# Kernel tuning notes

Measured on AMD Instinct MI355X. Metric: run time of the kernel, lower is better.

## Reference

```python
import jax, jax.numpy as jnp
import numpy as np
from jax.scipy.special import gammaln

EPS = 1e-8
N_SAMPLES = 2 ** 17
ATTACK_FULL_SIZE = 2048
CPD = 16
N_RES = 16
EXPR = 2
N_OSC = 2
N_GAUSS = 8
N_EVENTS = 4
FRAMES = 128
DEF_FRAMES = 128
N_LEVELS = 11  # log2(ATTACK_FULL_SIZE)


def unit_norm(x, axis=-1):
    return x / (jnp.linalg.norm(x, axis=axis, keepdims=True) + EPS)


def fft_convolve(a, b):
    # zero-pad to 2n to avoid circular wraparound, multiply spectra, crop to n
    n = a.shape[-1]
    fa = jnp.fft.rfft(a, n=2 * n, axis=-1)
    fb = jnp.fft.rfft(b, n=2 * n, axis=-1)
    return jnp.fft.irfft(fa * fb, n=2 * n, axis=-1)[..., :n]


def upsample_with_holes(x, size):
    # zero-insertion upsampling: place frames at stride `factor`
    factor = size // x.shape[-1]
    out = jnp.zeros(x.shape[:-1] + (size,), x.dtype)
    return out.at[..., ::factor].set(x)


def interpolate_last_axis(x, size):
    # linear interpolation, align_corners=False semantics (torch F.interpolate)
    n = x.shape[-1]
    scale = n / size
    src = jnp.clip((jnp.arange(size) + 0.5) * scale - 0.5, 0.0, n - 1.0)
    lo = jnp.floor(src).astype(jnp.int32)
    hi = jnp.minimum(lo + 1, n - 1)
    w = (src - lo).astype(x.dtype)
    return x[..., lo] * (1.0 - w) + x[..., hi] * w


def ensure_last_axis_length(x, size):
    n = x.shape[-1]
    if n == size:
        return x
    if n > size:
        return x[..., :size]
    return jnp.pad(x, [(0, 0)] * (x.ndim - 1) + [(0, size - n)])


def sparse_softmax(x):
    # hard one-hot forward, softmax straight-through backward
    sm = jax.nn.softmax(x, axis=-1)
    hard = jax.nn.one_hot(jnp.argmax(x, axis=-1), x.shape[-1], dtype=x.dtype)
    return hard + sm - jax.lax.stop_gradient(sm)


def hierarchical_dirac(p):
    # p: (..., L, 2) binary choices per level -> one-hot dirac of length 2**L
    sel = sparse_softmax(p)
    sig = sel[..., 0, :]
    for i in range(1, p.shape[-2]):
        sig = (sig[..., :, None] * sel[..., i, :][..., None, :]).reshape(*sig.shape[:-1], -1)
    return sig


def gamma_pdf(mean, std, n_elements):
    # gamma pdf on support (eps, 1], parameterized by mean/std
    t = jnp.linspace(EPS, 1.0, n_elements)
    k = (mean / (std + EPS)) ** 2
    rate = mean / (std ** 2 + EPS)
    k = k[..., None]
    rate = rate[..., None]
    logp = k * jnp.log(rate + EPS) + (k - 1.0) * jnp.log(t) - rate * t - gammaln(k)
    return jnp.exp(logp)


def damped_harmonic_oscillator(time, mass, damping, tension, x0):
    # underdamped closed-form solution, v0 = 0
    omega0_sq = tension / mass
    gamma = damping / (2.0 * mass)
    omega = jnp.sqrt(omega0_sq - gamma ** 2)
    A = x0
    B = gamma * x0 / omega
    return jnp.exp(-gamma * time) * (A * jnp.cos(omega * time) + B * jnp.sin(omega * time))


def dho_block(damping, mass, tension, disp, amps, tmod=None, scaling=None):
    time = jnp.linspace(0.0, 10.0, N_SAMPLES).reshape(1, 1, 1, N_SAMPLES)
    t = tension[..., None]  # (N_OSC, N_RES, EXPR, 1)
    if tmod is not None:
        t = t + tmod[0] * scaling  # broadcast -> (N_OSC, N_RES, EXPR, N_SAMPLES)
    x = damped_harmonic_oscillator(
        time,
        jax.nn.sigmoid(mass[..., None]) * 2.0,
        jax.nn.sigmoid(damping[..., None]) * 30.0,
        10.0 ** t,
        disp[..., None],
    )
    x = (x * amps).sum(axis=0)  # sum over oscillators
    return x.reshape(1, 1, N_RES, EXPR, N_SAMPLES)


def attack_envelopes(means, stds, amps, pos, overall_amp):
    m, s, a = jnp.abs(means), jnp.abs(stds), jnp.abs(amps)
    p = hierarchical_dirac(pos)  # (1,1,CPD,NG,2048)
    x = gamma_pdf(m, s, ATTACK_FULL_SIZE) * a[..., None]
    x = fft_convolve(x, p)
    x = x.sum(axis=2)  # (1,1,NG,2048)
    x = unit_norm(x)
    x = x * overall_amp[..., None]  # broadcast -> (1,1,CPD,NG,2048)
    x = x.sum(axis=-2)  # (1,1,CPD,2048)
    return x.reshape(CPD, ATTACK_FULL_SIZE)


def _forward(control_signal, deformations, ae_means, ae_stds, ae_amps, ae_pos,
             ae_overall_amp, dho_damping, dho_mass, dho_tension, dho_disp, dho_amp,
             influences, stack_mix, router, layer_mix, gains, attack_noise):
    b, ne, cpd, frames = control_signal.shape
    # --- DampedHarmonicOscillatorStack ---
    o1 = dho_block(dho_damping[0], dho_mass[0], dho_tension[0], dho_disp[0], dho_amp[0])
    o2 = dho_block(dho_damping[1], dho_mass[1], dho_tension[1], dho_disp[1], dho_amp[1], o1, influences[0])
    o3 = dho_block(dho_damping[2], dho_mass[2], dho_tension[2], dho_disp[2], dho_amp[2], o2, influences[1])
    res = (jnp.stack([o1, o2, o3], axis=-1) * jax.nn.softmax(stack_mix, axis=-1)).sum(axis=-1)
    res = unit_norm(res)
    # --- AttackEnvelopes ---
    ae = attack_envelopes(ae_means, ae_stds, ae_amps, ae_pos, ae_overall_amp)
    # --- execute_layer ---
    routed = jnp.einsum('becf,cr->berf', control_signal, router)
    before = routed
    res = unit_norm(res)  # execute_layer normalizes again
    routed = upsample_with_holes(routed.reshape(b, ne, N_RES, 1, frames), N_SAMPLES)
    # ae.shape[-1] == window_size, so materialize_attack_envelopes just multiplies noise
    impulse = ensure_last_axis_length(ae * attack_noise, N_SAMPLES).reshape(1, 1, cpd, 1, N_SAMPLES)
    routed = fft_convolve(impulse, routed)  # (1,ne,N_RES,1,S)
    cs = routed.reshape(1, ne, cpd, N_SAMPLES).sum(axis=1, keepdims=True)
    conv = fft_convolve(routed, res)  # (1,ne,N_RES,EXPR,S)
    base = jnp.zeros_like(deformations).at[:, :, 0:1, :].set(1.0)
    d = jax.nn.softmax(base + deformations, axis=-2)
    d = interpolate_last_axis(d.reshape(b, 1, 1, EXPR, -1), N_SAMPLES)
    x = (d * conv).sum(axis=-2)  # (1,ne,N_RES,S)
    mixes = jax.nn.softmax(layer_mix.reshape(1, 1, N_RES, 1, 1, 2), axis=-1)
    stacked = jnp.stack([routed, x.reshape(routed.shape)], axis=-1)
    x = (mixes * stacked).sum(axis=-1)
    x = x.reshape(1, 1, N_RES, -1)
    summed = jnp.tanh(x * jnp.abs(gains.reshape(1, 1, N_RES, 1)))
    summed = summed.sum(axis=-2, keepdims=True)
    return summed, before, cs


def setup_inputs() -> dict:
    key = jax.random.key(0)
    ks = jax.random.split(key, 20)
    u = lambda k, shape, lo, hi: jax.random.uniform(k, shape, jnp.float32, lo, hi)
    inp = {}
    inp['control_signal'] = jax.random.uniform(ks[0], (1, N_EVENTS, CPD, FRAMES), jnp.float32)
    inp['deformations'] = jax.random.normal(ks[1], (1, 1, EXPR, DEF_FRAMES), jnp.float32)
    inp['ae_means'] = u(ks[2], (1, 1, CPD, N_GAUSS), -6.0, 6.0)
    inp['ae_stds'] = u(ks[3], (1, 1, CPD, N_GAUSS), 0.5, 6.0)
    inp['ae_amps'] = u(ks[4], (1, 1, CPD, N_GAUSS), -6.0, 6.0)
    inp['ae_pos'] = u(ks[5], (1, 1, CPD, N_GAUSS, N_LEVELS, 2), -1.0, 1.0)
    inp['ae_overall_amp'] = u(ks[6], (1, 1, CPD, 1), -1.0, 1.0)
    inp['dho_damping'] = u(ks[7], (3, N_OSC, N_RES, EXPR), 0.5, 1.5)
    inp['dho_mass'] = u(ks[8], (3, N_OSC, N_RES, EXPR), -2.0, 2.0)
    inp['dho_tension'] = u(ks[9], (3, N_OSC, N_RES, EXPR), 4.0, 9.0)
    inp['dho_disp'] = u(ks[10], (3, N_OSC, N_RES, EXPR), -1.0, 2.0)
    inp['dho_amp'] = u(ks[11], (3, N_OSC, N_RES, EXPR, 1), -1.0, 1.0)
    inp['influences'] = u(ks[12], (2, N_OSC, N_RES, EXPR, 1), -0.01, 0.01)
    inp['stack_mix'] = u(ks[13], (1, 1, N_RES, EXPR, 1, 3), -1.0, 1.0)
    router = u(ks[14], (CPD, N_RES), -1.0, 1.0)
    mask = (jax.random.uniform(ks[15], (CPD, N_RES)) < 0.1).astype(jnp.float32)
    inp['router'] = router * mask
    inp['layer_mix'] = u(ks[16], (N_RES, 2), -1.0, 1.0)
    inp['gains'] = u(ks[17], (N_RES, 1), 0.01, 1.1)
    inp['attack_noise'] = u(ks[18], (CPD, ATTACK_FULL_SIZE), -1.0, 1.0)
    return inp


def reference(control_signal, deformations, ae_means, ae_stds, ae_amps, ae_pos,
              ae_overall_amp, dho_damping, dho_mass, dho_tension, dho_disp, dho_amp,
              influences, stack_mix, router, layer_mix, gains, attack_noise):
    return _forward(control_signal, deformations, ae_means, ae_stds, ae_amps, ae_pos,
                    ae_overall_amp, dho_damping, dho_mass, dho_tension, dho_disp, dho_amp,
                    influences, stack_mix, router, layer_mix, gains, attack_noise)
```

## Files before the change

### kernel.cpp

```cpp
#include <hip/hip_runtime.h>
#include <math.h>

#define NS 131072
#define EPSF 1e-8f

#define OFF_IMP    8388608u
#define OFF_VG     8421376u
#define OFF_DW     8437760u
#define OFF_FV     8568832u
#define OFF_NORM   8577024u
#define OFF_MIX0   8577064u
#define OFF_MIX1   8577080u
#define OFF_GABS   8577096u
#define OFF_PART   8578560u
#define OFF_GSSP   8594944u

#define AFRAG_USH  4194304u
#define ABF2_USH   4726784u
#define HB_USH     8388608u

typedef __attribute__((ext_vector_type(8))) short short8;
typedef __attribute__((ext_vector_type(4))) float floatx4;
typedef __attribute__((ext_vector_type(4))) unsigned short ushort4v;

#define INV2PI 0.15915494309189535f

__device__ __forceinline__ float sigmf(float x) { return 1.0f / (1.0f + expf(-x)); }

__device__ __forceinline__ unsigned short f2bf(float x) {
  unsigned u = __float_as_uint(x);
  unsigned r = (u + 0x7FFFu + ((u >> 16) & 1u)) >> 16;
  return (unsigned short)r;
}

__global__ __launch_bounds__(256) void k01_prep_dho(
    const float* __restrict__ csig, const float* __restrict__ deform,
    const float* __restrict__ ddmp, const float* __restrict__ dmas,
    const float* __restrict__ dten, const float* __restrict__ ddisp,
    const float* __restrict__ damp, const float* __restrict__ infl,
    const float* __restrict__ smix, const float* __restrict__ router,
    const float* __restrict__ lmix, const float* __restrict__ gains,
    const float* __restrict__ means, const float* __restrict__ stds,
    const float* __restrict__ amps, const float* __restrict__ pos,
    float* __restrict__ wsf, unsigned short* __restrict__ abf2,
    unsigned short* __restrict__ resb, float* __restrict__ partials,
    float* __restrict__ out)
{
  int tid = threadIdx.x;
  int bid = blockIdx.x;
  if (bid < 512) {
    int t = bid * 256 + tid;
    {
      float4 z = {0.f, 0.f, 0.f, 0.f};
      *(float4*)&out[(size_t)t * 4] = z;
    }
    {
      float src = (t + 0.5f) * (1.0f / 1024.0f) - 0.5f;
      src = fminf(fmaxf(src, 0.0f), 127.0f);
      int lo = (int)src;
      int hi = min(lo + 1, 127);
      float w = src - (float)lo;
      float c0l = 1.0f / (1.0f + expf(deform[128 + lo] - (1.0f + deform[lo])));
      float c0h = 1.0f / (1.0f + expf(deform[128 + hi] - (1.0f + deform[hi])));
      wsf[OFF_DW + t] = c0l * (1.0f - w) + c0h * w;
    }
    int mt = bid & 7, e = (bid >> 3) & 3, r = (bid >> 5) & 15;
    __shared__ float fvrow[128];
    if (tid < 128) {
      float s = 0.f;
      for (int c = 0; c < 16; ++c)
        s += csig[(e * 16 + c) * 128 + tid] * router[c * 16 + r];
      fvrow[tid] = s;
      if (mt == 0) {
        wsf[OFF_FV + (e * 16 + r) * 128 + tid] = s;
        out[524288 + (e * 16 + r) * 128 + tid] = s;
      }
    }
    __syncthreads();
    {
      int gid = bid * 256 + tid;
      int lane = gid & 63;
      int kt = (gid >> 6) & 3;
      int m = lane & 15, quad = lane >> 4;
      int base = mt * 16 + m - kt * 32 - quad * 8;
      short8 v;
#pragma unroll
      for (int j = 0; j < 8; ++j) {
        int f = base - j;
        unsigned short b = 0;
        if (f >= 0 && f < 128) b = f2bf(fvrow[f]);
        v[j] = (short)b;
      }
      *(short8*)&abf2[(size_t)gid * 8] = v;
    }
    if (bid == 0 && tid < 16) {
      int r2 = tid;
      float l0 = lmix[r2 * 2], l1 = lmix[r2 * 2 + 1];
      float mx = fmaxf(l0, l1);
      float e0 = expf(l0 - mx), e1 = expf(l1 - mx), inv = 1.0f / (e0 + e1);
      wsf[OFF_MIX0 + r2] = e0 * inv;
      wsf[OFF_MIX1 + r2] = e1 * inv;
      wsf[OFF_GABS + r2] = fabsf(gains[r2]);
    }
  } else if (bid < 576) {
    int gb = bid - 512;
    int g = gb >> 3;
    int i = (gb & 7) * 256 + tid;
    __shared__ float kS[16], rateS[16], logAS[16], aS[16];
    __shared__ int dS[16];
    __shared__ float red[4];
    if (tid < 16) {
      int c = tid, idx = c * 8 + g;
      double m = fabs((double)means[idx]);
      double s = fabs((double)stds[idx]);
      double k = m / (s + 1e-8); k = k * k;
      double rate = m / (s * s + 1e-8);
      double logA = k * log(rate + 1e-8) - lgamma(k);
      kS[c] = (float)k; rateS[c] = (float)rate; logAS[c] = (float)logA;
      aS[c] = fabsf(amps[idx]);
      int d = 0;
      for (int l = 0; l < 11; ++l) {
        float p0 = pos[(idx * 11 + l) * 2], p1 = pos[(idx * 11 + l) * 2 + 1];
        d = d * 2 + (p1 > p0 ? 1 : 0);
      }
      dS[c] = d;
    }
    __syncthreads();
    const float step = (float)((1.0 - 1e-8) / 2047.0);
    float v = 0.f;
    for (int c = 0; c < 16; ++c) {
      int mi = i - dS[c];
      if (mi >= 0) {
        float tm = 1e-8f + (float)mi * step;
        float lp = logAS[c] + (kS[c] - 1.0f) * __logf(tm) - rateS[c] * tm;
        v += aS[c] * __expf(lp);
      }
    }
    wsf[OFF_VG + g * 2048 + i] = v;
    float sumsq = v * v;
#pragma unroll
    for (int off = 32; off; off >>= 1) sumsq += __shfl_down(sumsq, off, 64);
    if ((tid & 63) == 0) red[tid >> 6] = sumsq;
    __syncthreads();
    if (tid == 0) wsf[OFF_GSSP + gb] = red[0] + red[1] + red[2] + red[3];
  } else {
    int b = bid - 576;
    int rx = b >> 9;
    int t = (b & 511) * 256 + tid;
    int r = rx >> 1, x = rx & 1;
    __shared__ float pf[40];
    __shared__ float bred[4];
    if (tid < 6) {
      int ent = tid, bb = ent >> 1, o = ent & 1;
      int id = ((bb * 2 + o) * 16 + r) * 2 + x;
      float mass = 2.0f * sigmf(dmas[id]);
      float gam = 30.0f * sigmf(ddmp[id]) / (2.0f * mass);
      double W = exp((double)dten[id] * 2.302585092994046) / (double)mass;
      float x0v = ddisp[id];
      float ampv = damp[id];
      float infv = 0.f;
      if (bb == 1) infv = infl[(o * 16 + r) * 2 + x];
      if (bb == 2) infv = infl[((2 + o) * 16 + r) * 2 + x];
      pf[0 + ent]  = -gam;
      pf[6 + ent]  = ampv * x0v;
      pf[12 + ent] = gam * ampv * x0v;
      pf[18 + ent] = infv * 2.3025851f;
      if (bb == 0) {
        double om = sqrt(W - (double)gam * (double)gam);
        pf[24 + o] = (float)((double)(gam * x0v * ampv) / om);
        pf[26 + o] = (float)(om * 0.15915494309189535);
      } else {
        pf[28 + ent - 2] = (float)W;
      }
    }
    if (tid == 8) {
      float a0 = smix[rx * 3], a1 = smix[rx * 3 + 1], a2 = smix[rx * 3 + 2];
      float mm = fmaxf(a0, fmaxf(a1, a2));
      float e0 = expf(a0 - mm), e1 = expf(a1 - mm), e2 = expf(a2 - mm);
      float inv = 1.0f / (e0 + e1 + e2);
      pf[33] = e0 * inv; pf[34] = e1 * inv; pf[35] = e2 * inv;
    }
    __syncthreads();
    float ttf = (float)t * (10.0f / 131071.0f);
    float o1v = 0.f;
#pragma unroll
    for (int o = 0; o < 2; ++o) {
      float fr = pf[26 + o] * ttf;
      fr -= rintf(fr);
      float sn = __builtin_amdgcn_sinf(fr);
      float cn = __builtin_amdgcn_cosf(fr);
      float ex = __expf(pf[o] * ttf);
      o1v += ex * (pf[6 + o] * cn + pf[24 + o] * sn);
    }
    float prev = o1v, o2v = 0.f, o3v = 0.f;
#pragma unroll
    for (int blk = 1; blk < 3; ++blk) {
      float acc = 0.f;
#pragma unroll
      for (int oo = 0; oo < 2; ++oo) {
        int o = blk * 2 + oo;
        float ng = pf[o];
        float p10 = __expf(prev * pf[18 + o]);
        float rad = __builtin_fmaf(pf[28 + o - 2], p10, -(ng * ng));
        float om = __builtin_amdgcn_sqrtf(rad);
        float fr = (om * INV2PI) * ttf;
        fr -= rintf(fr);
        float sn = __builtin_amdgcn_sinf(fr);
        float cn = __builtin_amdgcn_cosf(fr);
        float Bp = pf[12 + o] * __builtin_amdgcn_rcpf(om);
        float ex = __expf(ng * ttf);
        acc += ex * (pf[6 + o] * cn + Bp * sn);
      }
      if (blk == 1) o2v = acc; else o3v = acc;
      prev = acc;
    }
    float rv = pf[33] * o1v + pf[34] * o2v + pf[35] * o3v;
    resb[(size_t)rx * NS + t] = f2bf(rv);
    float sq = rv * rv;
#pragma unroll
    for (int off = 32; off; off >>= 1) sq += __shfl_down(sq, off, 64);
    if ((tid & 63) == 0) bred[tid >> 6] = sq;
    __syncthreads();
    if (tid == 0)
      partials[rx * 512 + (b & 511)] = bred[0] + bred[1] + bred[2] + bred[3];
  }
}

__global__ __launch_bounds__(256) void kB_mid(
    const float* __restrict__ ovamp, const float* __restrict__ noise,
    float* __restrict__ wsf, unsigned short* __restrict__ abf)
{
  int bid = blockIdx.x;
  int tid = threadIdx.x;
  if (bid < 32) {
    int rx = bid;
    const float* partials = wsf + OFF_PART;
    __shared__ float red[4];
    float s = partials[rx * 512 + tid] + partials[rx * 512 + 256 + tid];
#pragma unroll
    for (int off = 32; off; off >>= 1) s += __shfl_down(s, off, 64);
    if ((tid & 63) == 0) red[tid >> 6] = s;
    __syncthreads();
    if (tid == 0) wsf[OFF_NORM + rx] = red[0] + red[1] + red[2] + red[3];
    return;
  }
  __shared__ float wS[8];
  if (tid < 8) {
    float g8 = 0.f;
#pragma unroll
    for (int u = 0; u < 8; ++u) g8 += wsf[OFF_GSSP + tid * 8 + u];
    wS[tid] = 1.0f / (sqrtf(g8) + EPSF);
  }
  __syncthreads();
  const float* vg = wsf + OFF_VG;
  if (bid < 160) {
    int idx0 = bid - 32;
    int c = idx0 >> 3;
    int i = (idx0 & 7) * 256 + tid;
    float S = 0.f;
#pragma unroll
    for (int g = 0; g < 8; ++g) S += vg[g * 2048 + i] * wS[g];
    wsf[OFF_IMP + c * 2048 + i] = ovamp[c] * S * noise[c * 2048 + i];
    return;
  }
  int gid = (bid - 160) * 256 + tid;
  if (gid >= 66560) return;
  int r = gid / (65 * 64);
  int rem = gid % (65 * 64);
  int sc = rem >> 6, lane = rem & 63;
  int m = lane & 15, quad = lane >> 4;
  int qp = (quad < 2) ? quad : quad - 4;
  int base = 32 * sc + m - 8 * qp;
  float oa = ovamp[r];
  short8 v;
#pragma unroll
  for (int j = 0; j < 8; ++j) {
    int idx = base - j;
    unsigned short b = 0;
    if (idx >= 0 && idx < 2048) {
      float S = 0.f;
#pragma unroll
      for (int g = 0; g < 8; ++g) S += vg[g * 2048 + idx] * wS[g];
      b = f2bf(oa * S * noise[r * 2048 + idx]);
    }
    v[j] = (short)b;
  }
  *(short8*)&abf[(size_t)gid * 8] = v;
}

__global__ __launch_bounds__(256) void k4_mfma(
    const unsigned short* __restrict__ resb, const unsigned short* __restrict__ abf,
    const float* __restrict__ wsf, unsigned short* __restrict__ Hb)
{
  int rx = blockIdx.y, r = rx >> 1;
  int n0 = blockIdx.x * 256;
  __shared__ __align__(16) unsigned short Xs[9280];
  int tid = threadIdx.x;
  for (int i = tid; i < 772; i += 256) {
    int q_rel = i >> 1, p8 = (i & 1) * 8;
    int q = n0 - 130 + q_rel;
    short8 v = {0, 0, 0, 0, 0, 0, 0, 0};
    if (q >= 0) v = *(const short8*)&resb[(size_t)rx * NS + q * 16 + p8];
    *(short8*)&Xs[q_rel * 24 + p8] = v;
  }
  __syncthreads();
  int lane = tid & 63, w = tid >> 6;
  int quad = lane >> 4, nl = lane & 15;
  float n1 = sqrtf(wsf[OFF_NORM + rx]);
  float s1 = 1.0f / (n1 + EPSF);
  float scale = s1 * (1.0f / (n1 * s1 + EPSF)) * wsf[OFF_MIX1 + r];
  const short8* af = (const short8*)(abf) + (size_t)r * 65 * 64 + lane;
  floatx4 acc0 = {0,0,0,0}, acc1 = {0,0,0,0}, acc2 = {0,0,0,0}, acc3 = {0,0,0,0};
  const char* xbase = (const char*)Xs + (size_t)(130 + w * 64 + nl - (quad >> 1)) * 48
                      + (quad & 1) * 16;
  short8 wbuf[25];
#pragma unroll
  for (int s = -24; s < 0; ++s)
    wbuf[s + 25] = *(const short8*)(xbase - 96 * s);
#pragma unroll
  for (int sc = 0; sc < 65; ++sc) {
    wbuf[sc % 25] = *(const short8*)(xbase - 96 * sc);
    short8 a = af[sc * 64];
    acc0 = __builtin_amdgcn_mfma_f32_16x16x32_bf16(a, wbuf[sc % 25],        acc0, 0, 0, 0);
    acc1 = __builtin_amdgcn_mfma_f32_16x16x32_bf16(a, wbuf[(sc + 17) % 25], acc1, 0, 0, 0);
    acc2 = __builtin_amdgcn_mfma_f32_16x16x32_bf16(a, wbuf[(sc + 9) % 25],  acc2, 0, 0, 0);
    acc3 = __builtin_amdgcn_mfma_f32_16x16x32_bf16(a, wbuf[(sc + 1) % 25],  acc3, 0, 0, 0);
  }
  unsigned short* hp = Hb + (size_t)rx * NS + 16 * (n0 + w * 64 + nl) + quad * 4;
  ushort4v h0, h1, h2, h3;
#pragma unroll
  for (int i = 0; i < 4; ++i) {
    h0[i] = f2bf(acc0[i] * scale);
    h1[i] = f2bf(acc1[i] * scale);
    h2[i] = f2bf(acc2[i] * scale);
    h3[i] = f2bf(acc3[i] * scale);
  }
  *(ushort4v*)(hp)       = h0;
  *(ushort4v*)(hp + 256) = h1;
  *(ushort4v*)(hp + 512) = h2;
  *(ushort4v*)(hp + 768) = h3;
}

__global__ __launch_bounds__(256) void k6_mfma(
    const unsigned short* __restrict__ Hb, const float* __restrict__ imp,
    const unsigned short* __restrict__ abf2,
    const float* __restrict__ wsf, float* __restrict__ out)
{
  int r = blockIdx.y;
  int n0 = blockIdx.x * 32;
  int rm = r & 3, rq = r >> 2;
  int tid = threadIdx.x;
  int w = tid >> 6, lane = tid & 63;
  int wc = w & 1, wm = w >> 1;
  int quad = lane >> 4, n = lane & 15;
  int col = n0 + wc * 16 + n;

  __shared__ float fvs[4][128];
  for (int i = tid; i < 512; i += 256)
    fvs[i >> 7][i & 127] = wsf[OFF_FV + ((i >> 7) * 16 + r) * 128 + (i & 127)];
  __syncthreads();

  short8 bf0[4], bf1[4];
  const unsigned short* H0 = Hb + (size_t)(2 * r) * NS + col;
  const unsigned short* H1 = Hb + (size_t)(2 * r + 1) * NS + col;
#pragma unroll
  for (int kt = 0; kt < 4; ++kt) {
#pragma unroll
    for (int j = 0; j < 8; ++j) {
      int p = kt * 32 + quad * 8 + j;
      bf0[kt][j] = (short)H0[(size_t)p * 1024];
      bf1[kt][j] = (short)H1[(size_t)p * 1024];
    }
  }

  float d0r[4][4];
  const float* dwg = wsf + OFF_DW;
#pragma unroll
  for (int mi = 0; mi < 4; ++mi)
#pragma unroll
    for (int i = 0; i < 4; ++i) {
      int q = (wm * 4 + mi) * 16 + quad * 4 + i;
      d0r[mi][i] = dwg[q * 1024 + col];
    }

  float impA = imp[r * 2048 + col];
  float impB = imp[r * 2048 + 1024 + col];
  float mix0r = wsf[OFF_MIX0 + r];

  float tansum[4][4], csum[4][4];
#pragma unroll
  for (int mi = 0; mi < 4; ++mi)
#pragma unroll
    for (int i = 0; i < 4; ++i) { tansum[mi][i] = 0.f; csum[mi][i] = 0.f; }

  const short8* af = (const short8*)abf2;
  for (int e = 0; e < 4; ++e) {
    float ge = wsf[OFF_GABS + 4 * e + rq];
    const short8* afe = af + ((size_t)(r * 4 + e) * 32) * 64 + lane;
#pragma unroll
    for (int mi = 0; mi < 4; ++mi) {
      int mt = wm * 4 + mi;
      floatx4 acc0 = {0, 0, 0, 0}, acc1 = {0, 0, 0, 0};
#pragma unroll
      for (int kt = 0; kt < 4; ++kt) {
        short8 a = afe[(mt * 4 + kt) * 64];
        acc0 = __builtin_amdgcn_mfma_f32_16x16x32_bf16(a, bf0[kt], acc0, 0, 0, 0);
        acc1 = __builtin_amdgcn_mfma_f32_16x16x32_bf16(a, bf1[kt], acc1, 0, 0, 0);
      }
#pragma unroll
      for (int i = 0; i < 4; ++i) {
        int q = mt * 16 + quad * 4 + i;
        float fq = fvs[e][q];
        float fqm = (q > 0) ? fvs[e][q - 1] : 0.f;
        float rsv = fq * impA + fqm * impB;
        csum[mi][i] += rsv;
        float d0 = d0r[mi][i];
        float conv = d0 * acc0[i] + (1.0f - d0) * acc1[i];
        float z = (mix0r * rsv + conv) * ge;
        float e2 = __expf(2.0f * z);
        tansum[mi][i] += 1.0f - 2.0f * __builtin_amdgcn_rcpf(e2 + 1.0f);
      }
    }
  }
#pragma unroll
  for (int mi = 0; mi < 4; ++mi)
#pragma unroll
    for (int i = 0; i < 4; ++i) {
      int q = (wm * 4 + mi) * 16 + quad * 4 + i;
      atomicAdd(&out[(size_t)rm * NS + q * 1024 + col], tansum[mi][i]);
      out[532480 + (size_t)r * NS + q * 1024 + col] = csum[mi][i];
    }
}

extern "C" void kernel_launch(void* const* d_in, const int* in_sizes, int n_in,
                              void* d_out, int out_size, void* d_ws, size_t ws_size,
                              hipStream_t stream) {
  const float* csig   = (const float*)d_in[0];
  const float* deform = (const float*)d_in[1];
  const float* aem    = (const float*)d_in[2];
  const float* aes    = (const float*)d_in[3];
  const float* aea    = (const float*)d_in[4];
  const float* aep    = (const float*)d_in[5];
  const float* aeo    = (const float*)d_in[6];
  const float* ddmp   = (const float*)d_in[7];
  const float* dmas   = (const float*)d_in[8];
  const float* dten   = (const float*)d_in[9];
  const float* ddisp  = (const float*)d_in[10];
  const float* damp   = (const float*)d_in[11];
  const float* infl   = (const float*)d_in[12];
  const float* smix   = (const float*)d_in[13];
  const float* router = (const float*)d_in[14];
  const float* lmix   = (const float*)d_in[15];
  const float* gains  = (const float*)d_in[16];
  const float* anoise = (const float*)d_in[17];

  float*  wsf = (float*)d_ws;
  unsigned short* resb = (unsigned short*)d_ws;
  unsigned short* abf  = (unsigned short*)d_ws + AFRAG_USH;
  unsigned short* abf2 = (unsigned short*)d_ws + ABF2_USH;
  unsigned short* Hb   = (unsigned short*)d_ws + HB_USH;
  float*  out = (float*)d_out;

  k01_prep_dho<<<16960, 256, 0, stream>>>(csig, deform, ddmp, dmas, dten, ddisp,
                                          damp, infl, smix, router, lmix, gains,
                                          aem, aes, aea, aep, wsf, abf2, resb,
                                          wsf + OFF_PART, out);
  kB_mid<<<420, 256, 0, stream>>>(aeo, anoise, wsf, abf);
  k4_mfma<<<dim3(32, 32), 256, 0, stream>>>(resb, abf, wsf, Hb);
  k6_mfma<<<dim3(32, 16), 256, 0, stream>>>(Hb, wsf + OFF_IMP, abf2, wsf, out);
}
```

Measured before the change: 170.2 us.

## Stage H tile through LDS with vector loads and split k6 rows across grid z

The k6 kernel used to load B fragments from global memory with strided scalar 16-bit reads. It now loads them with coalesced 16-byte vector reads into a padded LDS transpose buffer and reads the fragments back as short8. The output row tiles are also split across a new grid z dimension of two, so each block handles half the M tiles. This doubles the block count for better occupancy and latency hiding. The cost is that the H tile staging is repeated in both z blocks.

```diff
diff --git a/kernel.cpp b/kernel.cpp
--- a/kernel.cpp
+++ b/kernel.cpp
@@ -341,6 +341,7 @@
   *(ushort4v*)(hp + 768) = h3;
 }
 
+#define HPAD 136
 __global__ __launch_bounds__(256) void k6_mfma(
     const unsigned short* __restrict__ Hb, const float* __restrict__ imp,
     const unsigned short* __restrict__ abf2,
@@ -348,38 +349,47 @@
 {
   int r = blockIdx.y;
   int n0 = blockIdx.x * 32;
+  int zz = blockIdx.z;
   int rm = r & 3, rq = r >> 2;
   int tid = threadIdx.x;
   int w = tid >> 6, lane = tid & 63;
   int wc = w & 1, wm = w >> 1;
   int quad = lane >> 4, n = lane & 15;
-  int col = n0 + wc * 16 + n;
+  int cl = wc * 16 + n;
+  int col = n0 + cl;
 
   __shared__ float fvs[4][128];
+  __shared__ __align__(16) unsigned short hs[2 * 32 * HPAD];
   for (int i = tid; i < 512; i += 256)
     fvs[i >> 7][i & 127] = wsf[OFF_FV + ((i >> 7) * 16 + r) * 128 + (i & 127)];
+  {
+    int rxs = tid >> 7, p = tid & 127;
+    const unsigned short* src = Hb + (size_t)(2 * r + rxs) * NS + (size_t)p * 1024 + n0;
+    unsigned short* dst = hs + rxs * 32 * HPAD + p;
+#pragma unroll
+    for (int b4 = 0; b4 < 4; ++b4) {
+      short8 v = *(const short8*)(src + b4 * 8);
+#pragma unroll
+      for (int c = 0; c < 8; ++c)
+        dst[(size_t)(b4 * 8 + c) * HPAD] = (unsigned short)v[c];
+    }
+  }
   __syncthreads();
 
   short8 bf0[4], bf1[4];
-  const unsigned short* H0 = Hb + (size_t)(2 * r) * NS + col;
-  const unsigned short* H1 = Hb + (size_t)(2 * r + 1) * NS + col;
 #pragma unroll
   for (int kt = 0; kt < 4; ++kt) {
-#pragma unroll
-    for (int j = 0; j < 8; ++j) {
-      int p = kt * 32 + quad * 8 + j;
-      bf0[kt][j] = (short)H0[(size_t)p * 1024];
-      bf1[kt][j] = (short)H1[(size_t)p * 1024];
-    }
-  }
-
-  float d0r[4][4];
+    bf0[kt] = *(const short8*)&hs[(0 * 32 + cl) * HPAD + kt * 32 + quad * 8];
+    bf1[kt] = *(const short8*)&hs[(1 * 32 + cl) * HPAD + kt * 32 + quad * 8];
+  }
+
+  float d0r[2][4];
   const float* dwg = wsf + OFF_DW;
 #pragma unroll
-  for (int mi = 0; mi < 4; ++mi)
+  for (int mi = 0; mi < 2; ++mi)
 #pragma unroll
     for (int i = 0; i < 4; ++i) {
-      int q = (wm * 4 + mi) * 16 + quad * 4 + i;
+      int q = (zz * 4 + wm * 2 + mi) * 16 + quad * 4 + i;
       d0r[mi][i] = dwg[q * 1024 + col];
     }
 
@@ -387,9 +397,9 @@
   float impB = imp[r * 2048 + 1024 + col];
   float mix0r = wsf[OFF_MIX0 + r];
 
-  float tansum[4][4], csum[4][4];
-#pragma unroll
-  for (int mi = 0; mi < 4; ++mi)
+  float tansum[2][4], csum[2][4];
+#pragma unroll
+  for (int mi = 0; mi < 2; ++mi)
 #pragma unroll
     for (int i = 0; i < 4; ++i) { tansum[mi][i] = 0.f; csum[mi][i] = 0.f; }
 
@@ -398,8 +408,8 @@
     float ge = wsf[OFF_GABS + 4 * e + rq];
     const short8* afe = af + ((size_t)(r * 4 + e) * 32) * 64 + lane;
 #pragma unroll
-    for (int mi = 0; mi < 4; ++mi) {
-      int mt = wm * 4 + mi;
+    for (int mi = 0; mi < 2; ++mi) {
+      int mt = zz * 4 + wm * 2 + mi;
       floatx4 acc0 = {0, 0, 0, 0}, acc1 = {0, 0, 0, 0};
 #pragma unroll
       for (int kt = 0; kt < 4; ++kt) {
@@ -423,10 +433,10 @@
     }
   }
 #pragma unroll
-  for (int mi = 0; mi < 4; ++mi)
+  for (int mi = 0; mi < 2; ++mi)
 #pragma unroll
     for (int i = 0; i < 4; ++i) {
-      int q = (wm * 4 + mi) * 16 + quad * 4 + i;
+      int q = (zz * 4 + wm * 2 + mi) * 16 + quad * 4 + i;
       atomicAdd(&out[(size_t)rm * NS + q * 1024 + col], tansum[mi][i]);
       out[532480 + (size_t)r * NS + q * 1024 + col] = csum[mi][i];
     }
@@ -467,5 +477,5 @@
                                           wsf + OFF_PART, out);
   kB_mid<<<420, 256, 0, stream>>>(aeo, anoise, wsf, abf);
   k4_mfma<<<dim3(32, 32), 256, 0, stream>>>(resb, abf, wsf, Hb);
-  k6_mfma<<<dim3(32, 16), 256, 0, stream>>>(Hb, wsf + OFF_IMP, abf2, wsf, out);
-}
+  k6_mfma<<<dim3(32, 16, 2), 256, 0, stream>>>(Hb, wsf + OFF_IMP, abf2, wsf, out);
+}
```

Result: no change. 169.8 us (-0.3%).
